# Performance work log

Measured on AMD Instinct MI355X. Metric: run time of the kernel, lower is better.

The kernel has to match this reference:

```python
import jax, jax.numpy as jnp
import numpy as np

NUM_HEADS = 8


def setup_inputs() -> dict:
    key = jax.random.key(0)
    k1, k2, k3 = jax.random.split(key, 3)
    B, N, C = 4, 2048, 768
    x = jax.random.normal(k1, (B, N, C), dtype=jnp.float32)
    proj_w = jax.random.normal(k2, (C, C), dtype=jnp.float32) * (C ** -0.5)
    proj_b = jax.random.normal(k3, (C,), dtype=jnp.float32) * 0.01
    return {"x": x, "proj_w": proj_w, "proj_b": proj_b}


def reference(x, proj_w, proj_b):
    B, N, C = x.shape
    H = NUM_HEADS
    d = C // H
    scale = d ** -0.5
    # NOTE: original forward ignores the qkv Linear; q = k = v = reshaped x.
    qkv = x.reshape(B, N, H, d).transpose(0, 2, 1, 3)  # (B, H, N, d)
    attn = jnp.einsum('bhnd,bhmd->bhnm', qkv, qkv) * scale  # (B, H, N, N)
    attn = jax.nn.softmax(attn, axis=-1)
    out = jnp.einsum('bhnm,bhmd->bhnd', attn, qkv)  # (B, H, N, d)
    out = out.transpose(0, 2, 1, 3).reshape(B, N, C)
    # nn.Linear: y = out @ W^T + b
    return out @ proj_w.T + proj_b
```

## Files before the change

kernel.cpp:

```cpp
#include <hip/hip_runtime.h>
#include <hip/hip_bf16.h>

#define B_ 4
#define N_ 2048
#define C_ 768
#define H_ 8
#define D_ 96

typedef __attribute__((ext_vector_type(8))) short bf16x8;
typedef __attribute__((ext_vector_type(4))) float f32x4;
typedef __attribute__((ext_vector_type(16))) float f32x16;
typedef __attribute__((ext_vector_type(4))) unsigned u32x4;

static __device__ __forceinline__ unsigned short bf16b(float f) {
  __hip_bfloat16 h = __float2bfloat16(f);
  return __builtin_bit_cast(unsigned short, h);
}
static __device__ __forceinline__ unsigned pack2(float a, float b) {
  return (unsigned)bf16b(a) | ((unsigned)bf16b(b) << 16);
}

__global__ __launch_bounds__(64) void k_prep(const float* __restrict__ x,
                                             __hip_bfloat16* __restrict__ Xbf,
                                             __hip_bfloat16* __restrict__ Vtg) {
  const int t = threadIdx.x;
  const int nc = blockIdx.x, bh = blockIdx.y;
  const int b = bh >> 3, h = bh & 7;
  const int n = nc * 64 + t;
  const size_t rowoff = ((size_t)(b * N_ + n)) * C_ + h * D_;
  const float* src = x + rowoff;
  __hip_bfloat16* dx = Xbf + rowoff;
#pragma unroll
  for (int c8 = 0; c8 < 12; ++c8) {
    float4 lo = *(const float4*)(src + c8 * 8);
    float4 hi = *(const float4*)(src + c8 * 8 + 4);
    unsigned short u0 = bf16b(lo.x), u1 = bf16b(lo.y), u2 = bf16b(lo.z), u3 = bf16b(lo.w);
    unsigned short u4 = bf16b(hi.x), u5 = bf16b(hi.y), u6 = bf16b(hi.z), u7 = bf16b(hi.w);
    uint4 pk;
    pk.x = (unsigned)u0 | ((unsigned)u1 << 16);
    pk.y = (unsigned)u2 | ((unsigned)u3 << 16);
    pk.z = (unsigned)u4 | ((unsigned)u5 << 16);
    pk.w = (unsigned)u6 | ((unsigned)u7 << 16);
    *(uint4*)(dx + c8 * 8) = pk;
    unsigned short uu[8] = {u0, u1, u2, u3, u4, u5, u6, u7};
#pragma unroll
    for (int e = 0; e < 8; ++e) {
      __hip_bfloat16 hv = __builtin_bit_cast(__hip_bfloat16, uu[e]);
      Vtg[((size_t)(bh * D_ + c8 * 8 + e)) * N_ + n] = hv;
    }
  }
}

__global__ __launch_bounds__(256) void k_castw(const float* __restrict__ w,
                                               __hip_bfloat16* __restrict__ Wbf) {
  const int i = blockIdx.x * 256 + threadIdx.x;
  float4 f = *(const float4*)(w + (size_t)i * 4);
  unsigned v0 = (unsigned)bf16b(f.x) | ((unsigned)bf16b(f.y) << 16);
  unsigned v1 = (unsigned)bf16b(f.z) | ((unsigned)bf16b(f.w) << 16);
  uint2 pk; pk.x = v0; pk.y = v1;
  *(uint2*)(Wbf + (size_t)i * 4) = pk;
}

static __device__ __forceinline__ bf16x8 scale8(bf16x8 v, float s) {
  bf16x8 r;
#pragma unroll
  for (int e = 0; e < 8; ++e) {
    __hip_bfloat16 hv = __builtin_bit_cast(__hip_bfloat16, (unsigned short)v[e]);
    r[e] = (short)bf16b(__bfloat162float(hv) * s);
  }
  return r;
}

__global__ __launch_bounds__(256, 3) void k_attn(const __hip_bfloat16* __restrict__ Xbf,
                                                 const __hip_bfloat16* __restrict__ Vtg,
                                                 __hip_bfloat16* __restrict__ Ybf) {
  __shared__ __hip_bfloat16 K2[2][64][104];
  __shared__ __hip_bfloat16 V2[2][96][72];

  const int tid = threadIdx.x;
  const int wid = tid >> 6, lane = tid & 63;
  const int lr = lane & 31, hi = lane >> 5;
  const int qt = blockIdx.x, bh = blockIdx.y;
  const int b = bh >> 3, h = bh & 7;
  const int q0w = qt * 128 + wid * 32;
  const float SL2E = 0.14724444f;

  bf16x8 qf[6];
  {
    const __hip_bfloat16* qp =
        Xbf + ((size_t)(b * N_ + q0w + lr)) * C_ + h * D_ + hi * 8;
#pragma unroll
    for (int kk = 0; kk < 6; ++kk)
      qf[kk] = scale8(*(const bf16x8*)(qp + kk * 16), SL2E);
  }

  const __hip_bfloat16* Kbase = Xbf + ((size_t)b * N_) * C_ + h * D_;
  const __hip_bfloat16* Vbase = Vtg + ((size_t)bh * D_) * N_;

  const __hip_bfloat16* gp[6];
  int lofs[6];
#pragma unroll
  for (int i = 0; i < 6; ++i) {
    if (i < 3) {
      int idx = tid + i * 256;
      int r = idx / 12, c = idx - r * 12;
      gp[i] = Kbase + (size_t)r * C_ + c * 8;
      lofs[i] = r * 104 + c * 8;
    } else {
      int j = tid + (i - 3) * 256;
      int r = j >> 3, c = j & 7;
      gp[i] = Vbase + (size_t)r * N_ + c * 8;
      lofs[i] = r * 72 + c * 8;
    }
  }
  bf16x8 sreg[6];
  auto stage_load = [&]() {
#pragma unroll
    for (int i = 0; i < 6; ++i) {
      sreg[i] = *(const bf16x8*)gp[i];
      gp[i] += (i < 3) ? 64 * C_ : 64;
    }
  };
  auto stage_write = [&](int buf) {
#pragma unroll
    for (int i = 0; i < 6; ++i) {
      if (i < 3)
        *(bf16x8*)(&K2[buf][0][0] + lofs[i]) = sreg[i];
      else
        *(bf16x8*)(&V2[buf][0][0] + lofs[i]) = sreg[i];
    }
  };

  f32x16 accO[3] = {};
  float lrun = 0.f;

  stage_load();
  stage_write(0);
  __syncthreads();

  int cur = 0;
  for (int kv0 = 0; kv0 < N_; kv0 += 64) {
    const bool more = (kv0 + 64) < N_;

    f32x16 accS[2] = {};
#pragma unroll
    for (int kk = 0; kk < 6; ++kk) {
#pragma unroll
      for (int tk = 0; tk < 2; ++tk) {
        bf16x8 kf = *(const bf16x8*)(&K2[cur][tk * 32 + lr][kk * 16 + hi * 8]);
        accS[tk] = __builtin_amdgcn_mfma_f32_32x32x16_bf16(kf, qf[kk], accS[tk], 0, 0, 0);
      }
    }

    if (more) stage_load();

    float psum = 0.f;
#pragma unroll
    for (int tk = 0; tk < 2; ++tk)
#pragma unroll
      for (int r = 0; r < 16; ++r) {
        float v = exp2f(accS[tk][r]);
        accS[tk][r] = v;
        psum += v;
      }
    lrun += psum;

    bf16x8 pbf[4];
#pragma unroll
    for (int tk = 0; tk < 2; ++tk) {
#pragma unroll
      for (int s = 0; s < 2; ++s) {
        unsigned lo0 = pack2(accS[tk][8 * s + 0], accS[tk][8 * s + 1]);
        unsigned lo1 = pack2(accS[tk][8 * s + 2], accS[tk][8 * s + 3]);
        unsigned hi0 = pack2(accS[tk][8 * s + 4], accS[tk][8 * s + 5]);
        unsigned hi1 = pack2(accS[tk][8 * s + 6], accS[tk][8 * s + 7]);
        asm volatile("v_permlane32_swap_b32 %0, %1" : "+v"(lo0), "+v"(hi0));
        asm volatile("v_permlane32_swap_b32 %0, %1" : "+v"(lo1), "+v"(hi1));
        u32x4 pw;
        pw.x = lo0; pw.y = lo1; pw.z = hi0; pw.w = hi1;
        pbf[tk * 2 + s] = __builtin_bit_cast(bf16x8, pw);
      }
    }

#pragma unroll
    for (int ks = 0; ks < 4; ++ks) {
#pragma unroll
      for (int dt = 0; dt < 3; ++dt) {
        bf16x8 va = *(const bf16x8*)(&V2[cur][dt * 32 + lr][ks * 16 + hi * 8]);
        accO[dt] = __builtin_amdgcn_mfma_f32_32x32x16_bf16(va, pbf[ks], accO[dt], 0, 0, 0);
      }
    }

    if (more) stage_write(cur ^ 1);
    __syncthreads();
    cur ^= 1;
  }

  float ltot = lrun + __shfl_xor(lrun, 32);
  float linv = 1.0f / ltot;
  __hip_bfloat16* yb =
      Ybf + ((size_t)(b * N_ + q0w + lr)) * C_ + h * D_ + hi * 4;
#pragma unroll
  for (int dt = 0; dt < 3; ++dt) {
#pragma unroll
    for (int rq = 0; rq < 4; ++rq) {
      ushort4 pk;
      pk.x = bf16b(accO[dt][rq * 4 + 0] * linv);
      pk.y = bf16b(accO[dt][rq * 4 + 1] * linv);
      pk.z = bf16b(accO[dt][rq * 4 + 2] * linv);
      pk.w = bf16b(accO[dt][rq * 4 + 3] * linv);
      *(ushort4*)(yb + dt * 32 + rq * 8) = pk;
    }
  }
}

__global__ __launch_bounds__(256) void k_proj(const __hip_bfloat16* __restrict__ Ybf,
                                              const __hip_bfloat16* __restrict__ Wbf,
                                              const float* __restrict__ bias,
                                              float* __restrict__ out) {
  __shared__ __hip_bfloat16 Alds[128][40];
  __shared__ __hip_bfloat16 Blds[128][40];
  const int tid = threadIdx.x, wid = tid >> 6, lane = tid & 63;
  const int lr = lane & 15, lg = lane >> 4;
  const int m0 = blockIdx.x * 128, n0 = blockIdx.y * 128;
  const int wm = (wid >> 1) * 64, wn = (wid & 1) * 64;

  const f32x4 fzero = {0.f, 0.f, 0.f, 0.f};
  f32x4 acc[4][4];
#pragma unroll
  for (int mi = 0; mi < 4; ++mi)
#pragma unroll
    for (int ni = 0; ni < 4; ++ni) acc[mi][ni] = fzero;

  for (int k0 = 0; k0 < C_; k0 += 32) {
#pragma unroll
    for (int i = 0; i < 2; ++i) {
      int idx = tid + i * 256;
      int r = idx >> 2, cc = idx & 3;
      *(bf16x8*)(&Alds[r][cc * 8]) =
          *(const bf16x8*)(Ybf + (size_t)(m0 + r) * C_ + k0 + cc * 8);
      *(bf16x8*)(&Blds[r][cc * 8]) =
          *(const bf16x8*)(Wbf + (size_t)(n0 + r) * C_ + k0 + cc * 8);
    }
    __syncthreads();
    bf16x8 af[4], bfr[4];
#pragma unroll
    for (int i = 0; i < 4; ++i) {
      af[i] = *(const bf16x8*)(&Alds[wm + i * 16 + lr][lg * 8]);
      bfr[i] = *(const bf16x8*)(&Blds[wn + i * 16 + lr][lg * 8]);
    }
#pragma unroll
    for (int mi = 0; mi < 4; ++mi)
#pragma unroll
      for (int ni = 0; ni < 4; ++ni)
        acc[mi][ni] = __builtin_amdgcn_mfma_f32_16x16x32_bf16(af[mi], bfr[ni], acc[mi][ni], 0, 0, 0);
    __syncthreads();
  }

#pragma unroll
  for (int mi = 0; mi < 4; ++mi) {
#pragma unroll
    for (int ni = 0; ni < 4; ++ni) {
      int col = n0 + wn + ni * 16 + lr;
      float bv = bias[col];
#pragma unroll
      for (int j = 0; j < 4; ++j) {
        int row = m0 + wm + mi * 16 + lg * 4 + j;
        out[(size_t)row * C_ + col] = acc[mi][ni][j] + bv;
      }
    }
  }
}

extern "C" void kernel_launch(void* const* d_in, const int* in_sizes, int n_in,
                              void* d_out, int out_size, void* d_ws, size_t ws_size,
                              hipStream_t stream) {
  const float* x = (const float*)d_in[0];
  const float* pw = (const float*)d_in[1];
  const float* pb = (const float*)d_in[2];
  float* out = (float*)d_out;

  __hip_bfloat16* Xbf = (__hip_bfloat16*)d_ws;
  __hip_bfloat16* Vtg = Xbf + (size_t)B_ * N_ * C_;
  __hip_bfloat16* Wbf = Vtg + (size_t)B_ * N_ * C_;
  __hip_bfloat16* Ybf = Wbf + (size_t)C_ * C_;

  k_prep<<<dim3(N_ / 64, B_ * H_), 64, 0, stream>>>(x, Xbf, Vtg);
  k_castw<<<(C_ * C_ / 4) / 256, 256, 0, stream>>>(pw, Wbf);
  k_attn<<<dim3(N_ / 128, B_ * H_), 256, 0, stream>>>(Xbf, Vtg, Ybf);
  k_proj<<<dim3((B_ * N_) / 128, C_ / 128), 256, 0, stream>>>(Ybf, Wbf, pb, out);
}
```

Before: 124.4 us.

## Split KV sequence across two wave groups in attention with LDS reduction

After: 225.7 us. 1.81x slower.

```diff
diff --git a/kernel.cpp b/kernel.cpp
--- a/kernel.cpp
+++ b/kernel.cpp
@@ -16,8 +16,10 @@
   __hip_bfloat16 h = __float2bfloat16(f);
   return __builtin_bit_cast(unsigned short, h);
 }
-static __device__ __forceinline__ unsigned pack2(float a, float b) {
-  return (unsigned)bf16b(a) | ((unsigned)bf16b(b) << 16);
+static __device__ __forceinline__ unsigned cvtpk(float lo, float hi) {
+  unsigned r;
+  asm("v_cvt_pk_bf16_f32 %0, %1, %2" : "=v"(r) : "v"(lo), "v"(hi));
+  return r;
 }
 
 __global__ __launch_bounds__(64) void k_prep(const float* __restrict__ x,
@@ -34,15 +36,17 @@
   for (int c8 = 0; c8 < 12; ++c8) {
     float4 lo = *(const float4*)(src + c8 * 8);
     float4 hi = *(const float4*)(src + c8 * 8 + 4);
-    unsigned short u0 = bf16b(lo.x), u1 = bf16b(lo.y), u2 = bf16b(lo.z), u3 = bf16b(lo.w);
-    unsigned short u4 = bf16b(hi.x), u5 = bf16b(hi.y), u6 = bf16b(hi.z), u7 = bf16b(hi.w);
     uint4 pk;
-    pk.x = (unsigned)u0 | ((unsigned)u1 << 16);
-    pk.y = (unsigned)u2 | ((unsigned)u3 << 16);
-    pk.z = (unsigned)u4 | ((unsigned)u5 << 16);
-    pk.w = (unsigned)u6 | ((unsigned)u7 << 16);
+    pk.x = cvtpk(lo.x, lo.y);
+    pk.y = cvtpk(lo.z, lo.w);
+    pk.z = cvtpk(hi.x, hi.y);
+    pk.w = cvtpk(hi.z, hi.w);
     *(uint4*)(dx + c8 * 8) = pk;
-    unsigned short uu[8] = {u0, u1, u2, u3, u4, u5, u6, u7};
+    unsigned short uu[8];
+    uu[0] = (unsigned short)(pk.x & 0xffff); uu[1] = (unsigned short)(pk.x >> 16);
+    uu[2] = (unsigned short)(pk.y & 0xffff); uu[3] = (unsigned short)(pk.y >> 16);
+    uu[4] = (unsigned short)(pk.z & 0xffff); uu[5] = (unsigned short)(pk.z >> 16);
+    uu[6] = (unsigned short)(pk.w & 0xffff); uu[7] = (unsigned short)(pk.w >> 16);
 #pragma unroll
     for (int e = 0; e < 8; ++e) {
       __hip_bfloat16 hv = __builtin_bit_cast(__hip_bfloat16, uu[e]);
@@ -55,34 +59,43 @@
                                                __hip_bfloat16* __restrict__ Wbf) {
   const int i = blockIdx.x * 256 + threadIdx.x;
   float4 f = *(const float4*)(w + (size_t)i * 4);
-  unsigned v0 = (unsigned)bf16b(f.x) | ((unsigned)bf16b(f.y) << 16);
-  unsigned v1 = (unsigned)bf16b(f.z) | ((unsigned)bf16b(f.w) << 16);
-  uint2 pk; pk.x = v0; pk.y = v1;
+  uint2 pk;
+  pk.x = cvtpk(f.x, f.y);
+  pk.y = cvtpk(f.z, f.w);
   *(uint2*)(Wbf + (size_t)i * 4) = pk;
 }
 
 static __device__ __forceinline__ bf16x8 scale8(bf16x8 v, float s) {
-  bf16x8 r;
+  float f[8];
 #pragma unroll
   for (int e = 0; e < 8; ++e) {
     __hip_bfloat16 hv = __builtin_bit_cast(__hip_bfloat16, (unsigned short)v[e]);
-    r[e] = (short)bf16b(__bfloat162float(hv) * s);
-  }
-  return r;
-}
-
-__global__ __launch_bounds__(256, 3) void k_attn(const __hip_bfloat16* __restrict__ Xbf,
+    f[e] = __bfloat162float(hv) * s;
+  }
+  u32x4 pw;
+  pw.x = cvtpk(f[0], f[1]);
+  pw.y = cvtpk(f[2], f[3]);
+  pw.z = cvtpk(f[4], f[5]);
+  pw.w = cvtpk(f[6], f[7]);
+  return __builtin_bit_cast(bf16x8, pw);
+}
+
+__global__ __launch_bounds__(512, 4) void k_attn(const __hip_bfloat16* __restrict__ Xbf,
                                                  const __hip_bfloat16* __restrict__ Vtg,
                                                  __hip_bfloat16* __restrict__ Ybf) {
-  __shared__ __hip_bfloat16 K2[2][64][104];
-  __shared__ __hip_bfloat16 V2[2][96][72];
+  __shared__ __align__(16) char smraw[54272];
+  short* Ks = (short*)smraw;
+  short* Vs = (short*)(smraw + 26624);
+  float* Osh = (float*)smraw;
+  float* lsh = (float*)(smraw + 49152);
 
   const int tid = threadIdx.x;
   const int wid = tid >> 6, lane = tid & 63;
+  const int qsub = wid & 3, grp = wid >> 2;
   const int lr = lane & 31, hi = lane >> 5;
   const int qt = blockIdx.x, bh = blockIdx.y;
   const int b = bh >> 3, h = bh & 7;
-  const int q0w = qt * 128 + wid * 32;
+  const int q0w = qt * 128 + qsub * 32;
   const float SL2E = 0.14724444f;
 
   bf16x8 qf[6];
@@ -94,86 +107,78 @@
       qf[kk] = scale8(*(const bf16x8*)(qp + kk * 16), SL2E);
   }
 
-  const __hip_bfloat16* Kbase = Xbf + ((size_t)b * N_) * C_ + h * D_;
-  const __hip_bfloat16* Vbase = Vtg + ((size_t)bh * D_) * N_;
-
-  const __hip_bfloat16* gp[6];
-  int lofs[6];
-#pragma unroll
-  for (int i = 0; i < 6; ++i) {
-    if (i < 3) {
-      int idx = tid + i * 256;
-      int r = idx / 12, c = idx - r * 12;
-      gp[i] = Kbase + (size_t)r * C_ + c * 8;
-      lofs[i] = r * 104 + c * 8;
-    } else {
-      int j = tid + (i - 3) * 256;
-      int r = j >> 3, c = j & 7;
-      gp[i] = Vbase + (size_t)r * N_ + c * 8;
-      lofs[i] = r * 72 + c * 8;
-    }
+  const short* Kbase = (const short*)(Xbf + ((size_t)b * N_) * C_ + h * D_);
+  const short* Vbase = (const short*)(Vtg + ((size_t)bh * D_) * N_);
+
+  const short* gk[3];
+  const short* gv[3];
+  int lko[3], lvo[3];
+#pragma unroll
+  for (int i = 0; i < 3; ++i) {
+    int idx = tid + i * 512;
+    int r = idx / 12, c = idx - r * 12;
+    gk[i] = Kbase + (size_t)r * C_ + c * 8;
+    lko[i] = r * 104 + c * 8;
+    int r2 = idx >> 4, c2 = idx & 15;
+    gv[i] = Vbase + (size_t)r2 * N_ + c2 * 8;
+    lvo[i] = ((c2 >> 3) * 96 + r2) * 72 + (c2 & 7) * 8;
   }
   bf16x8 sreg[6];
   auto stage_load = [&]() {
 #pragma unroll
-    for (int i = 0; i < 6; ++i) {
-      sreg[i] = *(const bf16x8*)gp[i];
-      gp[i] += (i < 3) ? 64 * C_ : 64;
+    for (int i = 0; i < 3; ++i) {
+      sreg[i] = *(const bf16x8*)gk[i];
+      gk[i] += 128 * C_;
+      sreg[3 + i] = *(const bf16x8*)gv[i];
+      gv[i] += 128;
     }
   };
-  auto stage_write = [&](int buf) {
-#pragma unroll
-    for (int i = 0; i < 6; ++i) {
-      if (i < 3)
-        *(bf16x8*)(&K2[buf][0][0] + lofs[i]) = sreg[i];
-      else
-        *(bf16x8*)(&V2[buf][0][0] + lofs[i]) = sreg[i];
+  auto stage_write = [&]() {
+#pragma unroll
+    for (int i = 0; i < 3; ++i) {
+      *(bf16x8*)(Ks + lko[i]) = sreg[i];
+      *(bf16x8*)(Vs + lvo[i]) = sreg[3 + i];
     }
   };
+
+  stage_load();
+  stage_write();
+  __syncthreads();
 
   f32x16 accO[3] = {};
   float lrun = 0.f;
-
-  stage_load();
-  stage_write(0);
-  __syncthreads();
-
-  int cur = 0;
-  for (int kv0 = 0; kv0 < N_; kv0 += 64) {
-    const bool more = (kv0 + 64) < N_;
-
-    f32x16 accS[2] = {};
-#pragma unroll
-    for (int kk = 0; kk < 6; ++kk) {
-#pragma unroll
-      for (int tk = 0; tk < 2; ++tk) {
-        bf16x8 kf = *(const bf16x8*)(&K2[cur][tk * 32 + lr][kk * 16 + hi * 8]);
-        accS[tk] = __builtin_amdgcn_mfma_f32_32x32x16_bf16(kf, qf[kk], accS[tk], 0, 0, 0);
-      }
-    }
-
-    if (more) stage_load();
-
-    float psum = 0.f;
-#pragma unroll
-    for (int tk = 0; tk < 2; ++tk)
+  const short* Kw = Ks + ((size_t)(grp * 64 + lr)) * 104 + hi * 8;
+  const short* Vw = Vs + ((size_t)(grp * 96 + lr)) * 72 + hi * 8;
+
+  for (int it = 0; it < N_ / 128; ++it) {
+    const bool more = it < (N_ / 128 - 1);
+
+    bf16x8 pbf[4];
+#pragma unroll
+    for (int tk = 0; tk < 2; ++tk) {
+      f32x16 accS = {};
+#pragma unroll
+      for (int kk = 0; kk < 6; ++kk) {
+        bf16x8 kf = *(const bf16x8*)(Kw + tk * 32 * 104 + kk * 16);
+        accS = __builtin_amdgcn_mfma_f32_32x32x16_bf16(kf, qf[kk], accS, 0, 0, 0);
+      }
+      if (tk == 0 && more) stage_load();
+
+      float psum = 0.f;
 #pragma unroll
       for (int r = 0; r < 16; ++r) {
-        float v = exp2f(accS[tk][r]);
-        accS[tk][r] = v;
+        float v = exp2f(accS[r]);
+        accS[r] = v;
         psum += v;
       }
-    lrun += psum;
-
-    bf16x8 pbf[4];
-#pragma unroll
-    for (int tk = 0; tk < 2; ++tk) {
+      lrun += psum;
+
 #pragma unroll
       for (int s = 0; s < 2; ++s) {
-        unsigned lo0 = pack2(accS[tk][8 * s + 0], accS[tk][8 * s + 1]);
-        unsigned lo1 = pack2(accS[tk][8 * s + 2], accS[tk][8 * s + 3]);
-        unsigned hi0 = pack2(accS[tk][8 * s + 4], accS[tk][8 * s + 5]);
-        unsigned hi1 = pack2(accS[tk][8 * s + 6], accS[tk][8 * s + 7]);
+        unsigned lo0 = cvtpk(accS[8 * s + 0], accS[8 * s + 1]);
+        unsigned lo1 = cvtpk(accS[8 * s + 2], accS[8 * s + 3]);
+        unsigned hi0 = cvtpk(accS[8 * s + 4], accS[8 * s + 5]);
+        unsigned hi1 = cvtpk(accS[8 * s + 6], accS[8 * s + 7]);
         asm volatile("v_permlane32_swap_b32 %0, %1" : "+v"(lo0), "+v"(hi0));
         asm volatile("v_permlane32_swap_b32 %0, %1" : "+v"(lo1), "+v"(hi1));
         u32x4 pw;
@@ -186,30 +191,52 @@
     for (int ks = 0; ks < 4; ++ks) {
 #pragma unroll
       for (int dt = 0; dt < 3; ++dt) {
-        bf16x8 va = *(const bf16x8*)(&V2[cur][dt * 32 + lr][ks * 16 + hi * 8]);
+        bf16x8 va = *(const bf16x8*)(Vw + dt * 32 * 72 + ks * 16);
         accO[dt] = __builtin_amdgcn_mfma_f32_32x32x16_bf16(va, pbf[ks], accO[dt], 0, 0, 0);
       }
     }
 
-    if (more) stage_write(cur ^ 1);
     __syncthreads();
-    cur ^= 1;
-  }
-
-  float ltot = lrun + __shfl_xor(lrun, 32);
-  float linv = 1.0f / ltot;
-  __hip_bfloat16* yb =
-      Ybf + ((size_t)(b * N_ + q0w + lr)) * C_ + h * D_ + hi * 4;
-#pragma unroll
-  for (int dt = 0; dt < 3; ++dt) {
-#pragma unroll
-    for (int rq = 0; rq < 4; ++rq) {
-      ushort4 pk;
-      pk.x = bf16b(accO[dt][rq * 4 + 0] * linv);
-      pk.y = bf16b(accO[dt][rq * 4 + 1] * linv);
-      pk.z = bf16b(accO[dt][rq * 4 + 2] * linv);
-      pk.w = bf16b(accO[dt][rq * 4 + 3] * linv);
-      *(ushort4*)(yb + dt * 32 + rq * 8) = pk;
+    if (more) {
+      stage_write();
+      __syncthreads();
+    }
+  }
+
+  if (grp == 0) {
+#pragma unroll
+    for (int dt = 0; dt < 3; ++dt)
+#pragma unroll
+      for (int r = 0; r < 16; ++r) {
+        int dloc = (r & 3) + 8 * (r >> 2) + 4 * hi;
+        Osh[(qsub * 96 + dt * 32 + dloc) * 32 + lr] = accO[dt][r];
+      }
+    lsh[qsub * 64 + lane] = lrun;
+  }
+  __syncthreads();
+  if (grp == 1) {
+    lrun += lsh[qsub * 64 + lane];
+    float ltot = lrun + __shfl_xor(lrun, 32);
+    float linv = 1.0f / ltot;
+    __hip_bfloat16* yb =
+        Ybf + ((size_t)(b * N_ + q0w + lr)) * C_ + h * D_ + hi * 4;
+#pragma unroll
+    for (int dt = 0; dt < 3; ++dt) {
+#pragma unroll
+      for (int rg = 0; rg < 4; ++rg) {
+        float v0 = (accO[dt][rg * 4 + 0] +
+                    Osh[(qsub * 96 + dt * 32 + 8 * rg + 4 * hi + 0) * 32 + lr]) * linv;
+        float v1 = (accO[dt][rg * 4 + 1] +
+                    Osh[(qsub * 96 + dt * 32 + 8 * rg + 4 * hi + 1) * 32 + lr]) * linv;
+        float v2 = (accO[dt][rg * 4 + 2] +
+                    Osh[(qsub * 96 + dt * 32 + 8 * rg + 4 * hi + 2) * 32 + lr]) * linv;
+        float v3 = (accO[dt][rg * 4 + 3] +
+                    Osh[(qsub * 96 + dt * 32 + 8 * rg + 4 * hi + 3) * 32 + lr]) * linv;
+        uint2 st;
+        st.x = cvtpk(v0, v1);
+        st.y = cvtpk(v2, v3);
+        *(uint2*)(yb + dt * 32 + rg * 8) = st;
+      }
     }
   }
 }
@@ -287,6 +314,6 @@
 
   k_prep<<<dim3(N_ / 64, B_ * H_), 64, 0, stream>>>(x, Xbf, Vtg);
   k_castw<<<(C_ * C_ / 4) / 256, 256, 0, stream>>>(pw, Wbf);
-  k_attn<<<dim3(N_ / 128, B_ * H_), 256, 0, stream>>>(Xbf, Vtg, Ybf);
+  k_attn<<<dim3(N_ / 128, B_ * H_), 512, 0, stream>>>(Xbf, Vtg, Ybf);
   k_proj<<<dim3((B_ * N_) / 128, C_ / 128), 256, 0, stream>>>(Ybf, Wbf, pb, out);
 }
```
